# Performance work log

Hardware: AMD Instinct MI355X
Metric: run time of the kernel (lower is better)

Reference implementation:

```python
import jax, jax.numpy as jnp
import numpy as np

WS = 7
NH = 4

def _rel_idx(ws):
    ch, cw = np.meshgrid(np.arange(ws), np.arange(ws), indexing='ij')
    cf = np.stack([ch.ravel(), cw.ravel()])  # [2, ws*ws]
    rel = cf[:, :, None] - cf[:, None, :]
    rel = rel.transpose(1, 2, 0)
    rel[:, :, 0] += ws - 1
    rel[:, :, 1] += ws - 1
    rel[:, :, 0] *= 2 * ws - 1
    return jnp.asarray(rel.sum(-1), dtype=jnp.int32)  # [N, N]

def layernorm(x, g, b, eps=1e-5):
    m = jnp.mean(x, -1, keepdims=True)
    v = jnp.var(x, -1, keepdims=True)
    return (x - m) * jax.lax.rsqrt(v + eps) * g + b

def setup_inputs() -> dict:
    key = jax.random.key(0)
    ks = jax.random.split(key, 8)
    B, HH, WW, C = 32, 56, 56, 128
    hid = 512
    s = 0.02
    return {
        'x': jax.random.normal(ks[0], (B, HH * WW, C), jnp.float32),
        'H': HH, 'W': WW,
        'norm1_g': jnp.ones((C,), jnp.float32),
        'norm1_b': jnp.zeros((C,), jnp.float32),
        'qkv_w': jax.random.normal(ks[1], (3 * C, C), jnp.float32) * s,
        'qkv_b': jnp.zeros((3 * C,), jnp.float32),
        'rel_bias_table': jax.random.normal(ks[2], ((2 * WS - 1) ** 2, NH), jnp.float32) * s,
        'rel_idx': _rel_idx(WS),
        'proj_w': jax.random.normal(ks[3], (C, C), jnp.float32) * s,
        'proj_b': jnp.zeros((C,), jnp.float32),
        'norm2_g': jnp.ones((C,), jnp.float32),
        'norm2_b': jnp.zeros((C,), jnp.float32),
        'mlp_w1': jax.random.normal(ks[4], (hid, C), jnp.float32) * s,
        'mlp_b1': jnp.zeros((hid,), jnp.float32),
        'mlp_w2': jax.random.normal(ks[5], (C, hid), jnp.float32) * s,
        'mlp_b2': jnp.zeros((C,), jnp.float32),
    }

def swin_block(x, H, W, norm1_g, norm1_b, qkv_w, qkv_b, rel_bias_table, rel_idx,
               proj_w, proj_b, norm2_g, norm2_b, mlp_w1, mlp_b1, mlp_w2, mlp_b2,
               shift=3, ws=WS, nh=NH):
    B, L, C = x.shape
    N = ws * ws
    hd = C // nh
    scale = hd ** -0.5
    shortcut = x
    h = layernorm(x, norm1_g, norm1_b).reshape(B, H, W, C)
    if shift > 0:
        h = jnp.roll(h, (-shift, -shift), axis=(1, 2))
    # window partition -> [B*nW, N, C]
    h = h.reshape(B, H // ws, ws, W // ws, ws, C).transpose(0, 1, 3, 2, 4, 5).reshape(-1, N, C)
    # attention (no mask in source forward)
    qkv = h @ qkv_w.T + qkv_b  # [B_, N, 3C]
    qkv = qkv.reshape(-1, N, 3, nh, hd).transpose(2, 0, 3, 1, 4)
    q, k, v = qkv[0] * scale, qkv[1], qkv[2]  # [B_, nh, N, hd]
    attn = jnp.einsum('bhnd,bhmd->bhnm', q, k)
    bias = rel_bias_table[rel_idx.reshape(-1)].reshape(N, N, nh).transpose(2, 0, 1)
    attn = jax.nn.softmax(attn + bias[None], axis=-1)
    o = jnp.einsum('bhnm,bhmd->bhnd', attn, v).transpose(0, 2, 1, 3).reshape(-1, N, C)
    o = o @ proj_w.T + proj_b
    # window reverse -> [B, H, W, C]
    o = o.reshape(B, H // ws, W // ws, ws, ws, C).transpose(0, 1, 3, 2, 4, 5).reshape(B, H, W, C)
    if shift > 0:
        o = jnp.roll(o, (shift, shift), axis=(1, 2))
    x = shortcut + o.reshape(B, L, C)
    h2 = layernorm(x, norm2_g, norm2_b)
    h2 = jax.nn.gelu(h2 @ mlp_w1.T + mlp_b1, approximate=False) @ mlp_w2.T + mlp_b2
    return x + h2

def reference(x, H, W, norm1_g, norm1_b, qkv_w, qkv_b, rel_bias_table, rel_idx,
              proj_w, proj_b, norm2_g, norm2_b, mlp_w1, mlp_b1, mlp_w2, mlp_b2):
    return swin_block(x, H, W, norm1_g, norm1_b, qkv_w, qkv_b, rel_bias_table, rel_idx,
                      proj_w, proj_b, norm2_g, norm2_b, mlp_w1, mlp_b1, mlp_w2, mlp_b2)
```

## Files before the change

kernel.cpp:

```cpp
#include <hip/hip_runtime.h>
#include <hip/hip_bf16.h>


#define NWIN 2048

typedef short short8  __attribute__((ext_vector_type(8)));
typedef short short4v __attribute__((ext_vector_type(4)));
typedef float f32x4   __attribute__((ext_vector_type(4)));

#define QKVW_OFF  0
#define PROJW_OFF 49152
#define W1_OFF    65536
#define W2_OFF    131072
#define BIAS_BYTE_OFF 393216

__device__ __forceinline__ short f2bs(float v) {
  __hip_bfloat16 h = __float2bfloat16(v);
  union { __hip_bfloat16 h; short s; } u; u.h = h; return u.s;
}
__device__ __forceinline__ float gelu_f(float v) {
  float u = v * (0.7978845608028654f + 0.03567740814f * v * v);
  return v * __builtin_amdgcn_rcpf(1.f + __expf(-2.f * u));
}

__global__ __launch_bounds__(256) void conv_kernel(
    const float* __restrict__ qkvw, const float* __restrict__ projw,
    const float* __restrict__ w1,   const float* __restrict__ w2,
    const float* __restrict__ tab,  const int* __restrict__ ridx,
    __hip_bfloat16* __restrict__ wsb, float* __restrict__ biasT)
{
  int idx = blockIdx.x * 256 + threadIdx.x;
  if (idx < 49152)       wsb[QKVW_OFF + idx]          = __float2bfloat16(qkvw[idx]);
  else if (idx < 65536)  wsb[PROJW_OFF + idx - 49152] = __float2bfloat16(projw[idx - 49152]);
  else if (idx < 131072) wsb[W1_OFF + idx - 65536]    = __float2bfloat16(w1[idx - 65536]);
  else if (idx < 196608) wsb[W2_OFF + idx - 131072]   = __float2bfloat16(w2[idx - 131072]);
  else if (idx < 212992) {
    int i = idx - 196608;
    int h = i >> 12, m = (i >> 6) & 63, n = i & 63;
    biasT[i] = (m < 49 && n < 49) ? tab[ridx[n*49 + m]*4 + h] : 0.f;
  }
}

__global__ __launch_bounds__(256, 2) void fused_kernel(
    const float* __restrict__ x,
    const float* __restrict__ n1g, const float* __restrict__ n1b,
    const __hip_bfloat16* __restrict__ qkvwb, const float* __restrict__ qkvb,
    const float* __restrict__ biasT,
    const __hip_bfloat16* __restrict__ projwb, const float* __restrict__ projb,
    const float* __restrict__ n2g, const float* __restrict__ n2b,
    const __hip_bfloat16* __restrict__ w1b, const float* __restrict__ b1,
    const __hip_bfloat16* __restrict__ w2b, const float* __restrict__ b2,
    float* __restrict__ out)
{
  __shared__ alignas(16) __hip_bfloat16 hbuf[64][136];
  __shared__ alignas(16) char regA[40960];
  __shared__ alignas(16) __hip_bfloat16 vT[4][32][72];
  __hip_bfloat16* const qkb = (__hip_bfloat16*)regA;
  float*          const x2s = (float*)regA;
  __hip_bfloat16* const hb  = (__hip_bfloat16*)regA;

  const int tid = threadIdx.x, wave = tid >> 6, lane = tid & 63;
  const int l15 = lane & 15, quad = lane >> 4;
  const int b = blockIdx.x >> 6, wi = (blockIdx.x >> 3) & 7, wj = blockIdx.x & 7;

  {
    float g0 = n1g[lane], g1 = n1g[lane+64], e0 = n1b[lane], e1 = n1b[lane+64];
    for (int n = wave; n < 49; n += 4) {
      int r = n / 7, c = n - r * 7;
      int si = wi*7 + r + 3; if (si >= 56) si -= 56;
      int sj = wj*7 + c + 3; if (sj >= 56) sj -= 56;
      const float* xr = x + (b*3136 + si*56 + sj) * 128;
      float v0 = xr[lane], v1 = xr[lane + 64];
      float s = v0 + v1, sq = v0*v0 + v1*v1;
      #pragma unroll
      for (int off = 32; off > 0; off >>= 1) {
        s  += __shfl_xor(s,  off);
        sq += __shfl_xor(sq, off);
      }
      float mean = s * 0.0078125f;
      float var  = sq * 0.0078125f - mean*mean;
      float rstd = rsqrtf(var + 1e-5f);
      hbuf[n][lane]    = __float2bfloat16((v0-mean)*rstd*g0 + e0);
      hbuf[n][lane+64] = __float2bfloat16((v1-mean)*rstd*g1 + e1);
    }
  }
  __syncthreads();

  {
    const int which = wave >> 1;
    const int fb    = (wave & 1) * 64;
    const int vb    = wave * 32;
    f32x4 asw[4][4] = {};
    f32x4 aor[4][2] = {};
    #pragma unroll
    for (int ks = 0; ks < 4; ++ks) {
      short8 hf[4];
      #pragma unroll
      for (int mt = 0; mt < 4; ++mt)
        hf[mt] = *(const short8*)(&hbuf[mt*16 + l15][ks*32 + quad*8]);
      #pragma unroll
      for (int ft = 0; ft < 4; ++ft) {
        short8 wf = *(const short8*)(qkvwb + (which*128 + fb + ft*16 + l15)*128 + ks*32 + quad*8);
        #pragma unroll
        for (int mt = 0; mt < 4; ++mt)
          asw[ft][mt] = __builtin_amdgcn_mfma_f32_16x16x32_bf16(wf, hf[mt], asw[ft][mt], 0, 0, 0);
      }
      #pragma unroll
      for (int nt = 0; nt < 2; ++nt) {
        short8 wf = *(const short8*)(qkvwb + (256 + vb + nt*16 + l15)*128 + ks*32 + quad*8);
        #pragma unroll
        for (int mt = 0; mt < 4; ++mt)
          aor[mt][nt] = __builtin_amdgcn_mfma_f32_16x16x32_bf16(hf[mt], wf, aor[mt][nt], 0, 0, 0);
      }
    }
    const float qs = (which == 0) ? 0.17677669529663687f : 1.0f;
    #pragma unroll
    for (int ft = 0; ft < 4; ++ft) {
      int fo = fb + ft*16 + quad*4;
      int hh = fo >> 5, d0 = fo & 31;
      float bb[4];
      #pragma unroll
      for (int r = 0; r < 4; ++r) bb[r] = qkvb[which*128 + fo + r];
      #pragma unroll
      for (int mt = 0; mt < 4; ++mt) {
        int m = mt*16 + l15;
        if (m < 49) {
          short4v pk;
          #pragma unroll
          for (int r = 0; r < 4; ++r) pk[r] = f2bs((asw[ft][mt][r] + bb[r]) * qs);
          *(short4v*)(qkb + ((hh*2 + which)*64 + m)*40 + d0) = pk;
        }
      }
    }
    #pragma unroll
    for (int nt = 0; nt < 2; ++nt) {
      int n = vb + nt*16 + l15;
      int hh = n >> 5, d = n & 31;
      float bia = qkvb[256 + n];
      #pragma unroll
      for (int mt = 0; mt < 4; ++mt) {
        int m0 = mt*16 + quad*4;
        short4v pk;
        #pragma unroll
        for (int r = 0; r < 4; ++r) {
          float v = (m0 + r < 49) ? (aor[mt][nt][r] + bia) : 0.f;
          pk[r] = f2bs(v);
        }
        *(short4v*)(&vT[hh][d][m0]) = pk;
      }
    }
  }
  __syncthreads();

  {
    const int h = wave;
    __hip_bfloat16* qbase = qkb + (h*2 + 0)*64*40;
    __hip_bfloat16* kbase = qkb + (h*2 + 1)*64*40;
    short8 kf[4], qf[4];
    #pragma unroll
    for (int mt = 0; mt < 4; ++mt) kf[mt] = *(const short8*)(kbase + (mt*16 + l15)*40 + quad*8);
    #pragma unroll
    for (int nt = 0; nt < 4; ++nt) qf[nt] = *(const short8*)(qbase + (nt*16 + l15)*40 + quad*8);
    f32x4 sacc[4][4] = {};
    #pragma unroll
    for (int mt = 0; mt < 4; ++mt)
      #pragma unroll
      for (int nt = 0; nt < 4; ++nt)
        sacc[mt][nt] = __builtin_amdgcn_mfma_f32_16x16x32_bf16(kf[mt], qf[nt], sacc[mt][nt], 0, 0, 0);

    const float* bT = biasT + h*4096;
    #pragma unroll
    for (int mt = 0; mt < 4; ++mt)
      #pragma unroll
      for (int nt = 0; nt < 4; ++nt)
        #pragma unroll
        for (int r = 0; r < 4; ++r)
          sacc[mt][nt][r] += bT[(mt*16 + quad*4 + r)*64 + nt*16 + l15];

    __hip_bfloat16* pb = qbase;
    #pragma unroll
    for (int nt = 0; nt < 4; ++nt) {
      float mx = -1e30f;
      #pragma unroll
      for (int mt = 0; mt < 3; ++mt)
        #pragma unroll
        for (int r = 0; r < 4; ++r) mx = fmaxf(mx, sacc[mt][nt][r]);
      mx = fmaxf(mx, (quad == 0) ? sacc[3][nt][0] : -1e30f);
      mx = fmaxf(mx, __shfl_xor(mx, 16));
      mx = fmaxf(mx, __shfl_xor(mx, 32));
      float sum = 0.f;
      #pragma unroll
      for (int mt = 0; mt < 3; ++mt)
        #pragma unroll
        for (int r = 0; r < 4; ++r) {
          float e = __expf(sacc[mt][nt][r] - mx);
          sacc[mt][nt][r] = e; sum += e;
        }
      {
        float e = (quad == 0) ? __expf(sacc[3][nt][0] - mx) : 0.f;
        sacc[3][nt][0] = e; sacc[3][nt][1] = 0.f; sacc[3][nt][2] = 0.f; sacc[3][nt][3] = 0.f;
        sum += e;
      }
      sum += __shfl_xor(sum, 16);
      sum += __shfl_xor(sum, 32);
      float inv = 1.f / sum;
      int n = nt*16 + l15;
      #pragma unroll
      for (int mt = 0; mt < 4; ++mt) {
        short4v pk;
        #pragma unroll
        for (int r = 0; r < 4; ++r) pk[r] = f2bs(sacc[mt][nt][r] * inv);
        *(short4v*)(pb + n*72 + mt*16 + quad*4) = pk;
      }
    }

    f32x4 oacc[2][4] = {};
    #pragma unroll
    for (int kt = 0; kt < 2; ++kt) {
      short8 vf[2], pf[4];
      #pragma unroll
      for (int dt = 0; dt < 2; ++dt)
        vf[dt] = *(const short8*)(&vT[h][dt*16 + l15][kt*32 + quad*8]);
      #pragma unroll
      for (int nc = 0; nc < 4; ++nc)
        pf[nc] = *(const short8*)(pb + (nc*16 + l15)*72 + kt*32 + quad*8);
      #pragma unroll
      for (int dt = 0; dt < 2; ++dt)
        #pragma unroll
        for (int nc = 0; nc < 4; ++nc)
          oacc[dt][nc] = __builtin_amdgcn_mfma_f32_16x16x32_bf16(vf[dt], pf[nc], oacc[dt][nc], 0, 0, 0);
    }
    #pragma unroll
    for (int dt = 0; dt < 2; ++dt)
      #pragma unroll
      for (int nc = 0; nc < 4; ++nc) {
        int n = nc*16 + l15;
        if (n < 49) {
          short4v pk;
          #pragma unroll
          for (int r = 0; r < 4; ++r) pk[r] = f2bs(oacc[dt][nc][r]);
          *(short4v*)(&hbuf[n][h*32 + dt*16 + quad*4]) = pk;
        }
      }
  }
  __syncthreads();

  f32x4 x2v[4][2];
  {
    const int ncol0 = wave * 32;
    f32x4 acc[4][2] = {};
    #pragma unroll
    for (int ks = 0; ks < 4; ++ks) {
      short8 af[4];
      #pragma unroll
      for (int mt = 0; mt < 4; ++mt)
        af[mt] = *(const short8*)(&hbuf[mt*16 + l15][ks*32 + quad*8]);
      #pragma unroll
      for (int nt = 0; nt < 2; ++nt) {
        short8 bf = *(const short8*)(projwb + (ncol0 + nt*16 + l15)*128 + ks*32 + quad*8);
        #pragma unroll
        for (int mt = 0; mt < 4; ++mt)
          acc[mt][nt] = __builtin_amdgcn_mfma_f32_16x16x32_bf16(af[mt], bf, acc[mt][nt], 0, 0, 0);
      }
    }
    #pragma unroll
    for (int nt = 0; nt < 2; ++nt) {
      int n = ncol0 + nt*16 + l15;
      float pbv = projb[n];
      #pragma unroll
      for (int mt = 0; mt < 4; ++mt) {
        #pragma unroll
        for (int r = 0; r < 4; ++r) {
          int m = mt*16 + quad*4 + r;
          float v = 0.f;
          if (m < 49) {
            int rr = m / 7, cc = m - rr * 7;
            int si = wi*7 + rr + 3; if (si >= 56) si -= 56;
            int sj = wj*7 + cc + 3; if (sj >= 56) sj -= 56;
            int o = (b*3136 + si*56 + sj) * 128 + n;
            v = acc[mt][nt][r] + pbv + x[o];
          }
          x2v[mt][nt][r] = v;
          x2s[m*132 + n] = v;
        }
      }
    }
  }
  __syncthreads();

  {
    float g0 = n2g[lane], g1 = n2g[lane+64], e0 = n2b[lane], e1 = n2b[lane+64];
    for (int n = wave; n < 49; n += 4) {
      float v0 = x2s[n*132 + lane], v1 = x2s[n*132 + lane + 64];
      float s = v0 + v1, sq = v0*v0 + v1*v1;
      #pragma unroll
      for (int off = 32; off > 0; off >>= 1) {
        s  += __shfl_xor(s,  off);
        sq += __shfl_xor(sq, off);
      }
      float mean = s * 0.0078125f;
      float var  = sq * 0.0078125f - mean*mean;
      float rstd = rsqrtf(var + 1e-5f);
      hbuf[n][lane]    = __float2bfloat16((v0-mean)*rstd*g0 + e0);
      hbuf[n][lane+64] = __float2bfloat16((v1-mean)*rstd*g1 + e1);
    }
    __hip_bfloat16 z = __float2bfloat16(0.f);
    for (int n = 49 + wave; n < 64; n += 4) {
      hbuf[n][lane] = z; hbuf[n][lane+64] = z;
    }
  }
  __syncthreads();

  f32x4 acc2[4][2] = {};
  #pragma unroll
  for (int chunk = 0; chunk < 2; ++chunk) {
    {
      const int jbl = wave * 64;
      const int jbg = chunk*256 + jbl;
      f32x4 acc1[4][4] = {};
      #pragma unroll
      for (int ks = 0; ks < 4; ++ks) {
        short8 lf[4];
        #pragma unroll
        for (int mt = 0; mt < 4; ++mt)
          lf[mt] = *(const short8*)(&hbuf[mt*16 + l15][ks*32 + quad*8]);
        #pragma unroll
        for (int jt = 0; jt < 4; ++jt) {
          short8 wf = *(const short8*)(w1b + (jbg + jt*16 + l15)*128 + ks*32 + quad*8);
          #pragma unroll
          for (int mt = 0; mt < 4; ++mt)
            acc1[jt][mt] = __builtin_amdgcn_mfma_f32_16x16x32_bf16(wf, lf[mt], acc1[jt][mt], 0, 0, 0);
        }
      }
      #pragma unroll
      for (int jt = 0; jt < 4; ++jt) {
        int j0l = jbl + jt*16 + quad*4;
        float bb[4];
        #pragma unroll
        for (int r = 0; r < 4; ++r) bb[r] = b1[chunk*256 + j0l + r];
        #pragma unroll
        for (int mt = 0; mt < 4; ++mt) {
          int m = mt*16 + l15;
          short4v pk;
          #pragma unroll
          for (int r = 0; r < 4; ++r) pk[r] = f2bs(gelu_f(acc1[jt][mt][r] + bb[r]));
          *(short4v*)(hb + m*264 + j0l) = pk;
        }
      }
    }
    __syncthreads();

    {
      const int fb2 = wave * 32;
      #pragma unroll
      for (int ks = 0; ks < 8; ++ks) {
        short8 af[4];
        #pragma unroll
        for (int mt = 0; mt < 4; ++mt)
          af[mt] = *(const short8*)(hb + (mt*16 + l15)*264 + ks*32 + quad*8);
        #pragma unroll
        for (int nt = 0; nt < 2; ++nt) {
          short8 bf = *(const short8*)(w2b + (fb2 + nt*16 + l15)*512 + chunk*256 + ks*32 + quad*8);
          #pragma unroll
          for (int mt = 0; mt < 4; ++mt)
            acc2[mt][nt] = __builtin_amdgcn_mfma_f32_16x16x32_bf16(af[mt], bf, acc2[mt][nt], 0, 0, 0);
        }
      }
    }
    if (chunk == 0) __syncthreads();
  }

  {
    const int fb2 = wave * 32;
    #pragma unroll
    for (int nt = 0; nt < 2; ++nt) {
      int f = fb2 + nt*16 + l15;
      float bb = b2[f];
      #pragma unroll
      for (int mt = 0; mt < 4; ++mt) {
        #pragma unroll
        for (int r = 0; r < 4; ++r) {
          int m = mt*16 + quad*4 + r;
          if (m < 49) {
            int rr = m / 7, cc = m - rr * 7;
            int si = wi*7 + rr + 3; if (si >= 56) si -= 56;
            int sj = wj*7 + cc + 3; if (sj >= 56) sj -= 56;
            int o = (b*3136 + si*56 + sj) * 128 + f;
            out[o] = acc2[mt][nt][r] + bb + x2v[mt][nt][r];
          }
        }
      }
    }
  }
}

extern "C" void kernel_launch(void* const* d_in, const int* in_sizes, int n_in,
                              void* d_out, int out_size, void* d_ws, size_t ws_size,
                              hipStream_t stream) {
  const float* x     = (const float*)d_in[0];
  const float* n1g   = (const float*)d_in[3];
  const float* n1b   = (const float*)d_in[4];
  const float* qkvw  = (const float*)d_in[5];
  const float* qkvb  = (const float*)d_in[6];
  const float* tab   = (const float*)d_in[7];
  const int*   ridx  = (const int*)d_in[8];
  const float* projw = (const float*)d_in[9];
  const float* projb = (const float*)d_in[10];
  const float* n2g   = (const float*)d_in[11];
  const float* n2b   = (const float*)d_in[12];
  const float* w1    = (const float*)d_in[13];
  const float* b1    = (const float*)d_in[14];
  const float* w2    = (const float*)d_in[15];
  const float* b2    = (const float*)d_in[16];
  float* outp = (float*)d_out;

  __hip_bfloat16* wsb = (__hip_bfloat16*)d_ws;
  float* biasT = (float*)((char*)d_ws + BIAS_BYTE_OFF);

  hipLaunchKernelGGL(conv_kernel, dim3(832), dim3(256), 0, stream,
                     qkvw, projw, w1, w2, tab, ridx, wsb, biasT);
  hipLaunchKernelGGL(fused_kernel, dim3(NWIN), dim3(256), 0, stream,
                     x, n1g, n1b, wsb + QKVW_OFF, qkvb, biasT, wsb + PROJW_OFF, projb,
                     n2g, n2b, wsb + W1_OFF, b1, wsb + W2_OFF, b2, outp);
}
```

Before: 302.6 us.

## Use 512-thread blocks and split each GEMM stage across 8 waves

Doubles the fused kernel's block size from 4 to 8 waves and repartitions every stage across them: QKV output tiles (3 per wave, uniform), attention split per head across two query halves, and the projection and MLP columns split into 16-wide slices per wave. The aim is more waves per CU for latency hiding and less accumulator state per wave, so register pressure drops. The V tile is now written transposed element by element instead of as packed vectors. An extra barrier is added in attention so the P tile can overwrite the Q buffer safely. The cost is more barrier participants and more redundant LDS fragment loads per block.

```diff
diff --git a/kernel.cpp b/kernel.cpp
--- a/kernel.cpp
+++ b/kernel.cpp
@@ -41,7 +41,7 @@
   }
 }
 
-__global__ __launch_bounds__(256, 2) void fused_kernel(
+__global__ __launch_bounds__(512, 4) void fused_kernel(
     const float* __restrict__ x,
     const float* __restrict__ n1g, const float* __restrict__ n1b,
     const __hip_bfloat16* __restrict__ qkvwb, const float* __restrict__ qkvb,
@@ -65,7 +65,7 @@
 
   {
     float g0 = n1g[lane], g1 = n1g[lane+64], e0 = n1b[lane], e1 = n1b[lane+64];
-    for (int n = wave; n < 49; n += 4) {
+    for (int n = wave; n < 49; n += 8) {
       int r = n / 7, c = n - r * 7;
       int si = wi*7 + r + 3; if (si >= 56) si -= 56;
       int sj = wj*7 + c + 3; if (sj >= 56) sj -= 56;
@@ -87,11 +87,8 @@
   __syncthreads();
 
   {
-    const int which = wave >> 1;
-    const int fb    = (wave & 1) * 64;
-    const int vb    = wave * 32;
-    f32x4 asw[4][4] = {};
-    f32x4 aor[4][2] = {};
+    const int t0 = wave * 3;
+    f32x4 acc[3][4] = {};
     #pragma unroll
     for (int ks = 0; ks < 4; ++ks) {
       short8 hf[4];
@@ -99,87 +96,85 @@
       for (int mt = 0; mt < 4; ++mt)
         hf[mt] = *(const short8*)(&hbuf[mt*16 + l15][ks*32 + quad*8]);
       #pragma unroll
-      for (int ft = 0; ft < 4; ++ft) {
-        short8 wf = *(const short8*)(qkvwb + (which*128 + fb + ft*16 + l15)*128 + ks*32 + quad*8);
+      for (int ft = 0; ft < 3; ++ft) {
+        short8 wf = *(const short8*)(qkvwb + ((t0 + ft)*16 + l15)*128 + ks*32 + quad*8);
         #pragma unroll
         for (int mt = 0; mt < 4; ++mt)
-          asw[ft][mt] = __builtin_amdgcn_mfma_f32_16x16x32_bf16(wf, hf[mt], asw[ft][mt], 0, 0, 0);
-      }
-      #pragma unroll
-      for (int nt = 0; nt < 2; ++nt) {
-        short8 wf = *(const short8*)(qkvwb + (256 + vb + nt*16 + l15)*128 + ks*32 + quad*8);
-        #pragma unroll
-        for (int mt = 0; mt < 4; ++mt)
-          aor[mt][nt] = __builtin_amdgcn_mfma_f32_16x16x32_bf16(hf[mt], wf, aor[mt][nt], 0, 0, 0);
-      }
-    }
-    const float qs = (which == 0) ? 0.17677669529663687f : 1.0f;
-    #pragma unroll
-    for (int ft = 0; ft < 4; ++ft) {
-      int fo = fb + ft*16 + quad*4;
-      int hh = fo >> 5, d0 = fo & 31;
-      float bb[4];
-      #pragma unroll
-      for (int r = 0; r < 4; ++r) bb[r] = qkvb[which*128 + fo + r];
-      #pragma unroll
-      for (int mt = 0; mt < 4; ++mt) {
-        int m = mt*16 + l15;
-        if (m < 49) {
-          short4v pk;
+          acc[ft][mt] = __builtin_amdgcn_mfma_f32_16x16x32_bf16(wf, hf[mt], acc[ft][mt], 0, 0, 0);
+      }
+    }
+    #pragma unroll
+    for (int ft = 0; ft < 3; ++ft) {
+      const int t = t0 + ft;
+      if (t < 16) {
+        const int which = t >> 3;
+        const int fo = (t & 7) * 16 + quad * 4;
+        const int hh = fo >> 5, d0 = fo & 31;
+        const float qs = (t < 8) ? 0.17677669529663687f : 1.0f;
+        float bb[4];
+        #pragma unroll
+        for (int r = 0; r < 4; ++r) bb[r] = qkvb[which*128 + fo + r];
+        #pragma unroll
+        for (int mt = 0; mt < 4; ++mt) {
+          int m = mt*16 + l15;
+          if (m < 49) {
+            short4v pk;
+            #pragma unroll
+            for (int r = 0; r < 4; ++r) pk[r] = f2bs((acc[ft][mt][r] + bb[r]) * qs);
+            *(short4v*)(qkb + ((hh*2 + which)*64 + m)*40 + d0) = pk;
+          }
+        }
+      } else {
+        const int nf = (t - 16) * 16 + quad * 4;
+        const int hh = nf >> 5, d0 = nf & 31;
+        float bb[4];
+        #pragma unroll
+        for (int r = 0; r < 4; ++r) bb[r] = qkvb[256 + nf + r];
+        #pragma unroll
+        for (int mt = 0; mt < 4; ++mt) {
+          int m = mt*16 + l15;
           #pragma unroll
-          for (int r = 0; r < 4; ++r) pk[r] = f2bs((asw[ft][mt][r] + bb[r]) * qs);
-          *(short4v*)(qkb + ((hh*2 + which)*64 + m)*40 + d0) = pk;
-        }
-      }
-    }
-    #pragma unroll
-    for (int nt = 0; nt < 2; ++nt) {
-      int n = vb + nt*16 + l15;
-      int hh = n >> 5, d = n & 31;
-      float bia = qkvb[256 + n];
-      #pragma unroll
-      for (int mt = 0; mt < 4; ++mt) {
-        int m0 = mt*16 + quad*4;
-        short4v pk;
-        #pragma unroll
-        for (int r = 0; r < 4; ++r) {
-          float v = (m0 + r < 49) ? (aor[mt][nt][r] + bia) : 0.f;
-          pk[r] = f2bs(v);
-        }
-        *(short4v*)(&vT[hh][d][m0]) = pk;
+          for (int r = 0; r < 4; ++r) {
+            float v = (m < 49) ? (acc[ft][mt][r] + bb[r]) : 0.f;
+            vT[hh][d0 + r][m] = __float2bfloat16(v);
+          }
+        }
       }
     }
   }
   __syncthreads();
 
   {
-    const int h = wave;
+    const int h = wave >> 1, half = wave & 1;
     __hip_bfloat16* qbase = qkb + (h*2 + 0)*64*40;
     __hip_bfloat16* kbase = qkb + (h*2 + 1)*64*40;
-    short8 kf[4], qf[4];
+    short8 kf[4], qf[2];
     #pragma unroll
     for (int mt = 0; mt < 4; ++mt) kf[mt] = *(const short8*)(kbase + (mt*16 + l15)*40 + quad*8);
     #pragma unroll
-    for (int nt = 0; nt < 4; ++nt) qf[nt] = *(const short8*)(qbase + (nt*16 + l15)*40 + quad*8);
-    f32x4 sacc[4][4] = {};
+    for (int nt = 0; nt < 2; ++nt)
+      qf[nt] = *(const short8*)(qbase + ((half*2 + nt)*16 + l15)*40 + quad*8);
+    __syncthreads();
+
+    f32x4 sacc[4][2] = {};
     #pragma unroll
     for (int mt = 0; mt < 4; ++mt)
       #pragma unroll
-      for (int nt = 0; nt < 4; ++nt)
+      for (int nt = 0; nt < 2; ++nt)
         sacc[mt][nt] = __builtin_amdgcn_mfma_f32_16x16x32_bf16(kf[mt], qf[nt], sacc[mt][nt], 0, 0, 0);
 
     const float* bT = biasT + h*4096;
     #pragma unroll
     for (int mt = 0; mt < 4; ++mt)
       #pragma unroll
-      for (int nt = 0; nt < 4; ++nt)
+      for (int nt = 0; nt < 2; ++nt)
         #pragma unroll
         for (int r = 0; r < 4; ++r)
-          sacc[mt][nt][r] += bT[(mt*16 + quad*4 + r)*64 + nt*16 + l15];
+          sacc[mt][nt][r] += bT[(mt*16 + quad*4 + r)*64 + (half*2 + nt)*16 + l15];
 
     __hip_bfloat16* pb = qbase;
     #pragma unroll
-    for (int nt = 0; nt < 4; ++nt) {
+    for (int nt = 0; nt < 2; ++nt) {
       float mx = -1e30f;
       #pragma unroll
       for (int mt = 0; mt < 3; ++mt)
@@ -204,7 +199,7 @@
       sum += __shfl_xor(sum, 16);
       sum += __shfl_xor(sum, 32);
       float inv = 1.f / sum;
-      int n = nt*16 + l15;
+      int n = (half*2 + nt)*16 + l15;
       #pragma unroll
       for (int mt = 0; mt < 4; ++mt) {
         short4v pk;
@@ -214,27 +209,27 @@
       }
     }
 
-    f32x4 oacc[2][4] = {};
+    f32x4 oacc[2][2] = {};
     #pragma unroll
     for (int kt = 0; kt < 2; ++kt) {
-      short8 vf[2], pf[4];
+      short8 vf[2], pf[2];
       #pragma unroll
       for (int dt = 0; dt < 2; ++dt)
         vf[dt] = *(const short8*)(&vT[h][dt*16 + l15][kt*32 + quad*8]);
       #pragma unroll
-      for (int nc = 0; nc < 4; ++nc)
-        pf[nc] = *(const short8*)(pb + (nc*16 + l15)*72 + kt*32 + quad*8);
+      for (int nc = 0; nc < 2; ++nc)
+        pf[nc] = *(const short8*)(pb + ((half*2 + nc)*16 + l15)*72 + kt*32 + quad*8);
       #pragma unroll
       for (int dt = 0; dt < 2; ++dt)
         #pragma unroll
-        for (int nc = 0; nc < 4; ++nc)
+        for (int nc = 0; nc < 2; ++nc)
           oacc[dt][nc] = __builtin_amdgcn_mfma_f32_16x16x32_bf16(vf[dt], pf[nc], oacc[dt][nc], 0, 0, 0);
     }
     #pragma unroll
     for (int dt = 0; dt < 2; ++dt)
       #pragma unroll
-      for (int nc = 0; nc < 4; ++nc) {
-        int n = nc*16 + l15;
+      for (int nc = 0; nc < 2; ++nc) {
+        int n = (half*2 + nc)*16 + l15;
         if (n < 49) {
           short4v pk;
           #pragma unroll
@@ -245,44 +240,38 @@
   }
   __syncthreads();
 
-  f32x4 x2v[4][2];
-  {
-    const int ncol0 = wave * 32;
-    f32x4 acc[4][2] = {};
+  f32x4 x2v[4];
+  {
+    const int ncol0 = wave * 16;
+    f32x4 acc[4] = {};
     #pragma unroll
     for (int ks = 0; ks < 4; ++ks) {
       short8 af[4];
       #pragma unroll
       for (int mt = 0; mt < 4; ++mt)
         af[mt] = *(const short8*)(&hbuf[mt*16 + l15][ks*32 + quad*8]);
-      #pragma unroll
-      for (int nt = 0; nt < 2; ++nt) {
-        short8 bf = *(const short8*)(projwb + (ncol0 + nt*16 + l15)*128 + ks*32 + quad*8);
-        #pragma unroll
-        for (int mt = 0; mt < 4; ++mt)
-          acc[mt][nt] = __builtin_amdgcn_mfma_f32_16x16x32_bf16(af[mt], bf, acc[mt][nt], 0, 0, 0);
-      }
-    }
-    #pragma unroll
-    for (int nt = 0; nt < 2; ++nt) {
-      int n = ncol0 + nt*16 + l15;
-      float pbv = projb[n];
-      #pragma unroll
-      for (int mt = 0; mt < 4; ++mt) {
-        #pragma unroll
-        for (int r = 0; r < 4; ++r) {
-          int m = mt*16 + quad*4 + r;
-          float v = 0.f;
-          if (m < 49) {
-            int rr = m / 7, cc = m - rr * 7;
-            int si = wi*7 + rr + 3; if (si >= 56) si -= 56;
-            int sj = wj*7 + cc + 3; if (sj >= 56) sj -= 56;
-            int o = (b*3136 + si*56 + sj) * 128 + n;
-            v = acc[mt][nt][r] + pbv + x[o];
-          }
-          x2v[mt][nt][r] = v;
-          x2s[m*132 + n] = v;
-        }
+      short8 bfr = *(const short8*)(projwb + (ncol0 + l15)*128 + ks*32 + quad*8);
+      #pragma unroll
+      for (int mt = 0; mt < 4; ++mt)
+        acc[mt] = __builtin_amdgcn_mfma_f32_16x16x32_bf16(af[mt], bfr, acc[mt], 0, 0, 0);
+    }
+    int n = ncol0 + l15;
+    float pbv = projb[n];
+    #pragma unroll
+    for (int mt = 0; mt < 4; ++mt) {
+      #pragma unroll
+      for (int r = 0; r < 4; ++r) {
+        int m = mt*16 + quad*4 + r;
+        float v = 0.f;
+        if (m < 49) {
+          int rr = m / 7, cc = m - rr * 7;
+          int si = wi*7 + rr + 3; if (si >= 56) si -= 56;
+          int sj = wj*7 + cc + 3; if (sj >= 56) sj -= 56;
+          int o = (b*3136 + si*56 + sj) * 128 + n;
+          v = acc[mt][r] + pbv + x[o];
+        }
+        x2v[mt][r] = v;
+        x2s[m*132 + n] = v;
       }
     }
   }
@@ -290,7 +279,7 @@
 
   {
     float g0 = n2g[lane], g1 = n2g[lane+64], e0 = n2b[lane], e1 = n2b[lane+64];
-    for (int n = wave; n < 49; n += 4) {
+    for (int n = wave; n < 49; n += 8) {
       float v0 = x2s[n*132 + lane], v1 = x2s[n*132 + lane + 64];
       float s = v0 + v1, sq = v0*v0 + v1*v1;
       #pragma unroll
@@ -305,19 +294,18 @@
       hbuf[n][lane+64] = __float2bfloat16((v1-mean)*rstd*g1 + e1);
     }
     __hip_bfloat16 z = __float2bfloat16(0.f);
-    for (int n = 49 + wave; n < 64; n += 4) {
+    for (int n = 49 + wave; n < 64; n += 8) {
       hbuf[n][lane] = z; hbuf[n][lane+64] = z;
     }
   }
   __syncthreads();
 
-  f32x4 acc2[4][2] = {};
+  f32x4 acc2[4] = {};
   #pragma unroll
   for (int chunk = 0; chunk < 2; ++chunk) {
     {
-      const int jbl = wave * 64;
-      const int jbg = chunk*256 + jbl;
-      f32x4 acc1[4][4] = {};
+      const int jbl = wave * 32;
+      f32x4 acc1[2][4] = {};
       #pragma unroll
       for (int ks = 0; ks < 4; ++ks) {
         short8 lf[4];
@@ -325,15 +313,15 @@
         for (int mt = 0; mt < 4; ++mt)
           lf[mt] = *(const short8*)(&hbuf[mt*16 + l15][ks*32 + quad*8]);
         #pragma unroll
-        for (int jt = 0; jt < 4; ++jt) {
-          short8 wf = *(const short8*)(w1b + (jbg + jt*16 + l15)*128 + ks*32 + quad*8);
+        for (int jt = 0; jt < 2; ++jt) {
+          short8 wf = *(const short8*)(w1b + (chunk*256 + jbl + jt*16 + l15)*128 + ks*32 + quad*8);
           #pragma unroll
           for (int mt = 0; mt < 4; ++mt)
             acc1[jt][mt] = __builtin_amdgcn_mfma_f32_16x16x32_bf16(wf, lf[mt], acc1[jt][mt], 0, 0, 0);
         }
       }
       #pragma unroll
-      for (int jt = 0; jt < 4; ++jt) {
+      for (int jt = 0; jt < 2; ++jt) {
         int j0l = jbl + jt*16 + quad*4;
         float bb[4];
         #pragma unroll
@@ -351,43 +339,36 @@
     __syncthreads();
 
     {
-      const int fb2 = wave * 32;
+      const int fb2 = wave * 16;
       #pragma unroll
       for (int ks = 0; ks < 8; ++ks) {
         short8 af[4];
         #pragma unroll
         for (int mt = 0; mt < 4; ++mt)
           af[mt] = *(const short8*)(hb + (mt*16 + l15)*264 + ks*32 + quad*8);
-        #pragma unroll
-        for (int nt = 0; nt < 2; ++nt) {
-          short8 bf = *(const short8*)(w2b + (fb2 + nt*16 + l15)*512 + chunk*256 + ks*32 + quad*8);
-          #pragma unroll
-          for (int mt = 0; mt < 4; ++mt)
-            acc2[mt][nt] = __builtin_amdgcn_mfma_f32_16x16x32_bf16(af[mt], bf, acc2[mt][nt], 0, 0, 0);
-        }
+        short8 bfr = *(const short8*)(w2b + (fb2 + l15)*512 + chunk*256 + ks*32 + quad*8);
+        #pragma unroll
+        for (int mt = 0; mt < 4; ++mt)
+          acc2[mt] = __builtin_amdgcn_mfma_f32_16x16x32_bf16(af[mt], bfr, acc2[mt], 0, 0, 0);
       }
     }
     if (chunk == 0) __syncthreads();
   }
 
   {
-    const int fb2 = wave * 32;
-    #pragma unroll
-    for (int nt = 0; nt < 2; ++nt) {
-      int f = fb2 + nt*16 + l15;
-      float bb = b2[f];
-      #pragma unroll
-      for (int mt = 0; mt < 4; ++mt) {
-        #pragma unroll
-        for (int r = 0; r < 4; ++r) {
-          int m = mt*16 + quad*4 + r;
-          if (m < 49) {
-            int rr = m / 7, cc = m - rr * 7;
-            int si = wi*7 + rr + 3; if (si >= 56) si -= 56;
-            int sj = wj*7 + cc + 3; if (sj >= 56) sj -= 56;
-            int o = (b*3136 + si*56 + sj) * 128 + f;
-            out[o] = acc2[mt][nt][r] + bb + x2v[mt][nt][r];
-          }
+    const int f = wave * 16 + l15;
+    const float bb = b2[f];
+    #pragma unroll
+    for (int mt = 0; mt < 4; ++mt) {
+      #pragma unroll
+      for (int r = 0; r < 4; ++r) {
+        int m = mt*16 + quad*4 + r;
+        if (m < 49) {
+          int rr = m / 7, cc = m - rr * 7;
+          int si = wi*7 + rr + 3; if (si >= 56) si -= 56;
+          int sj = wj*7 + cc + 3; if (sj >= 56) sj -= 56;
+          int o = (b*3136 + si*56 + sj) * 128 + f;
+          out[o] = acc2[mt][r] + bb + x2v[mt][r];
         }
       }
     }
@@ -419,7 +400,7 @@
 
   hipLaunchKernelGGL(conv_kernel, dim3(832), dim3(256), 0, stream,
                      qkvw, projw, w1, w2, tab, ridx, wsb, biasT);
-  hipLaunchKernelGGL(fused_kernel, dim3(NWIN), dim3(256), 0, stream,
+  hipLaunchKernelGGL(fused_kernel, dim3(NWIN), dim3(512), 0, stream,
                      x, n1g, n1b, wsb + QKVW_OFF, qkvb, biasT, wsb + PROJW_OFF, projb,
                      n2g, n2b, wsb + W1_OFF, b1, wsb + W2_OFF, b2, outp);
 }
```

Result: faster. 268.8 us (-11.2%).
